# Kernel optimization log

Hardware: AMD Instinct MI355X
Metric: run time of the kernel (lower is better)

The kernel has to match this reference:

```python
import jax, jax.numpy as jnp
import numpy as np

B, S, D, H, L, V = 2, 512, 1024, 16, 12, 50257
HD = D // H
DFF = 4 * D


def _ln(x, g, b, eps=1e-5):
    m = jnp.mean(x, axis=-1, keepdims=True)
    v = jnp.var(x, axis=-1, keepdims=True)
    return (x - m) * jax.lax.rsqrt(v + eps) * g + b


def setup_inputs() -> dict:
    key = jax.random.key(0)
    ks = jax.random.split(key, 32)
    sc = 0.02
    n = lambda k, shape: (jax.random.normal(k, shape, dtype=jnp.float32) * sc)
    inp = {
        "input_ids": jax.random.randint(ks[0], (B, S), 0, V, dtype=jnp.int64),
        "attention_mask": jnp.ones((B, S), dtype=jnp.float32),
        "image_hidden_states": jax.random.normal(ks[1], (B, D), dtype=jnp.float32),
        # token embedding table (also used for position embeds and tied lm_head, as in source)
        "wte": n(ks[2], (V, D)),
        # feature_space_transformation_nn: Linear(1024,1024) -> ReLU -> Linear(1024,1024)
        "ft_W1": n(ks[3], (D, D)), "ft_b1": jnp.zeros((D,), jnp.float32),
        "ft_W2": n(ks[4], (D, D)), "ft_b2": jnp.zeros((D,), jnp.float32),
        # per-layer params, stacked on leading L dim
        "ln1_g": jnp.ones((L, D), jnp.float32), "ln1_b": jnp.zeros((L, D), jnp.float32),
        "Wattn": n(ks[5], (L, D, 3 * D)), "battn": jnp.zeros((L, 3 * D), jnp.float32),
        "Wuk": n(ks[6], (L, D, D)), "buk": jnp.zeros((L, D), jnp.float32),
        "Wuv": n(ks[7], (L, D, D)), "buv": jnp.zeros((L, D), jnp.float32),
        "Wproj": n(ks[8], (L, D, D)), "bproj": jnp.zeros((L, D), jnp.float32),
        "ln2_g": jnp.ones((L, D), jnp.float32), "ln2_b": jnp.zeros((L, D), jnp.float32),
        "Wfc": n(ks[9], (L, D, DFF)), "bfc": jnp.zeros((L, DFF), jnp.float32),
        "Wfc2": n(ks[10], (L, DFF, D)), "bfc2": jnp.zeros((L, D), jnp.float32),
        "lnf_g": jnp.ones((D,), jnp.float32), "lnf_b": jnp.zeros((D,), jnp.float32),
    }
    return inp


def _forward(input_ids, attention_mask, image_hidden_states, wte,
             ft_W1, ft_b1, ft_W2, ft_b2,
             ln1_g, ln1_b, Wattn, battn, Wuk, buk, Wuv, buv, Wproj, bproj,
             ln2_g, ln2_b, Wfc, bfc, Wfc2, bfc2, lnf_g, lnf_b):
    # image feature transformation: Linear -> ReLU -> Linear
    img = jax.nn.relu(image_hidden_states @ ft_W1 + ft_b1) @ ft_W2 + ft_b2  # [B,D]

    # NOTE: source uses wte (not wpe) for position embeddings — faithful reproduction
    h = wte[input_ids] + wte[jnp.arange(S)][None]  # [B,S,D]

    # extended attention mask with a prepended zero column for the image token
    mask_ext = (1.0 - attention_mask)[:, None, None, :] * -10000.0  # [B,1,1,S]
    mask_ext = jnp.concatenate([jnp.zeros((B, 1, 1, 1), mask_ext.dtype), mask_ext], axis=-1)  # [B,1,1,S+1]

    # causal mask over kv_len=S+1: query i sees keys j <= i+1 (image token always visible)
    causal = jnp.arange(S + 1)[None, :] <= (jnp.arange(S)[:, None] + 1)  # [S,S+1]

    def block(h, p):
        (l1g, l1b, Wa, ba, Wk, bk, Wv, bv, Wp, bp, l2g, l2b, Wf, bf, Wf2, bf2) = p
        x = _ln(h, l1g, l1b)
        qkv = x @ Wa + ba
        q, k, v = jnp.split(qkv, 3, axis=-1)  # each [B,S,D]
        ki = (img @ Wk + bk)[:, None, :]  # [B,1,D]
        vi = (img @ Wv + bv)[:, None, :]
        k = jnp.concatenate([ki, k], axis=1)  # [B,S+1,D]
        v = jnp.concatenate([vi, v], axis=1)
        sh = lambda t, n: t.reshape(B, n, H, HD).transpose(0, 2, 1, 3)
        qh, kh, vh = sh(q, S), sh(k, S + 1), sh(v, S + 1)
        s = jnp.einsum('bhqd,bhkd->bhqk', qh, kh) / jnp.sqrt(jnp.float32(HD))
        s = jnp.where(causal[None, None], s, jnp.float32(-10000.0))
        s = s + mask_ext
        a = jax.nn.softmax(s, axis=-1)
        o = jnp.einsum('bhqk,bhkd->bhqd', a, vh).transpose(0, 2, 1, 3).reshape(B, S, D)
        h = h + (o @ Wp + bp)
        x = _ln(h, l2g, l2b)
        h = h + (jax.nn.gelu(x @ Wf + bf, approximate=True) @ Wf2 + bf2)
        return h, None

    params = (ln1_g, ln1_b, Wattn, battn, Wuk, buk, Wuv, buv, Wproj, bproj,
              ln2_g, ln2_b, Wfc, bfc, Wfc2, bfc2)
    h, _ = jax.lax.scan(block, h, params)
    h = _ln(h, lnf_g, lnf_b)
    return h @ wte.T  # tied lm head -> [B,S,V]


def reference(input_ids, attention_mask, image_hidden_states, wte,
              ft_W1, ft_b1, ft_W2, ft_b2,
              ln1_g, ln1_b, Wattn, battn, Wuk, buk, Wuv, buv, Wproj, bproj,
              ln2_g, ln2_b, Wfc, bfc, Wfc2, bfc2, lnf_g, lnf_b):
    return _forward(input_ids, attention_mask, image_hidden_states, wte,
                    ft_W1, ft_b1, ft_W2, ft_b2,
                    ln1_g, ln1_b, Wattn, battn, Wuk, buk, Wuv, buv, Wproj, bproj,
                    ln2_g, ln2_b, Wfc, bfc, Wfc2, bfc2, lnf_g, lnf_b)
```

## Files before the change

kernel.cpp:

```cpp
#include <hip/hip_runtime.h>
#include <cstdint>


typedef __bf16 bf16x8 __attribute__((ext_vector_type(8)));
typedef __bf16 bf16x4 __attribute__((ext_vector_type(4)));
typedef float  f32x4  __attribute__((ext_vector_type(4)));

#define GLDS16(g, l) __builtin_amdgcn_global_load_lds( \
    (const __attribute__((address_space(1))) unsigned int*)(g), \
    (__attribute__((address_space(3))) unsigned int*)(l), 16, 0, 0)

#define SCHED_FENCE() __builtin_amdgcn_sched_barrier(0)

__device__ __forceinline__ float gelu_f(float x) {
    float u = 1.5957691216057308f * (x + 0.044715f * x * x * x);
    float e = __expf(u);
    float t = 1.0f - 2.0f / (e + 1.0f);
    return 0.5f * x * (1.0f + t);
}

__device__ __forceinline__ int fragoff(int row, int kh, int hi) {
    return row * 64 + ((kh * 32 + hi * 8) ^ ((row & 7) << 3));
}

__device__ __forceinline__ void tcvt_body(
    int id, const float* __restrict__ Wa, const float* __restrict__ Wp,
    const float* __restrict__ Wf, const float* __restrict__ Wf2,
    __bf16* __restrict__ oa, __bf16* __restrict__ op,
    __bf16* __restrict__ of, __bf16* __restrict__ of2, float* tile)
{
    const float* src; __bf16* dst; int K, N, kb, nb;
    if (id < 768)       { src = Wa;  dst = oa;  K = 1024; N = 3072; kb = id & 15; nb = id >> 4; }
    else if (id < 1024) { id -= 768;  src = Wp;  dst = op;  K = 1024; N = 1024; kb = id & 15; nb = id >> 4; }
    else if (id < 2048) { id -= 1024; src = Wf;  dst = of;  K = 1024; N = 4096; kb = id & 15; nb = id >> 4; }
    else                { id -= 2048; src = Wf2; dst = of2; K = 4096; N = 1024; kb = id & 63; nb = id >> 6; }
    const int k0 = kb * 64, n0 = nb * 64;
    const int t = threadIdx.x;
    #pragma unroll
    for (int i = 0; i < 4; i++) {
        int r = i * 16 + (t >> 4), c = (t & 15) * 4;
        float4 v = *reinterpret_cast<const float4*>(src + (long)(k0 + r) * N + n0 + c);
        tile[r * 65 + c] = v.x; tile[r * 65 + c + 1] = v.y;
        tile[r * 65 + c + 2] = v.z; tile[r * 65 + c + 3] = v.w;
    }
    __syncthreads();
    const int nrow = t >> 2, kc = (t & 3) * 16;
    bf16x8 o0, o1;
    #pragma unroll
    for (int i = 0; i < 8; i++) {
        o0[i] = (__bf16)tile[(kc + i) * 65 + nrow];
        o1[i] = (__bf16)tile[(kc + 8 + i) * 65 + nrow];
    }
    *reinterpret_cast<bf16x8*>(dst + (long)(n0 + nrow) * K + k0 + kc)     = o0;
    *reinterpret_cast<bf16x8*>(dst + (long)(n0 + nrow) * K + k0 + kc + 8) = o1;
}

__device__ __forceinline__ void wcvt_body(
    int id, const float* __restrict__ wte, __bf16* __restrict__ out, long nvalid)
{
    long base = (long)id * 8192 + threadIdx.x * 8;
    #pragma unroll
    for (int i = 0; i < 4; i++) {
        long e = base + (long)i * 2048;
        bf16x8 o;
        if (e < nvalid) {
            float4 a = *reinterpret_cast<const float4*>(wte + e);
            float4 b = *reinterpret_cast<const float4*>(wte + e + 4);
            o[0] = (__bf16)a.x; o[1] = (__bf16)a.y; o[2] = (__bf16)a.z; o[3] = (__bf16)a.w;
            o[4] = (__bf16)b.x; o[5] = (__bf16)b.y; o[6] = (__bf16)b.z; o[7] = (__bf16)b.w;
        } else {
            #pragma unroll
            for (int q = 0; q < 8; q++) o[q] = (__bf16)0.f;
        }
        *reinterpret_cast<bf16x8*>(out + e) = o;
    }
}

__global__ __launch_bounds__(256) void tcvt_std(
    const float* __restrict__ Wa, const float* __restrict__ Wp,
    const float* __restrict__ Wf, const float* __restrict__ Wf2,
    __bf16* __restrict__ oa, __bf16* __restrict__ op,
    __bf16* __restrict__ of, __bf16* __restrict__ of2)
{
    __shared__ float tile[64 * 65];
    tcvt_body(blockIdx.x, Wa, Wp, Wf, Wf2, oa, op, of, of2, tile);
}

__global__ __launch_bounds__(256) void wcvt_std(
    const float* __restrict__ wte, __bf16* __restrict__ out, long nvalid)
{
    wcvt_body(blockIdx.x, wte, out, nvalid);
}

__global__ __launch_bounds__(256) void gemv_part(
    const float* __restrict__ x, int xld,
    const float* __restrict__ W, long wzs,
    float* __restrict__ part, int K, int N)
{
    int jb = blockIdx.x, kz = blockIdx.y, z = blockIdx.z;
    int t = threadIdx.x;
    int j = (jb << 6) + (t & 63);
    int g = t >> 6;
    int klen = K / (gridDim.y * 4);
    int kbase = (kz * 4 + g) * klen;
    const float* Wp = W + (long)z * wzs + (long)kbase * N + j;
    const float* x0 = x + kbase;
    const float* x1 = x + xld + kbase;
    float a0 = 0.f, a1 = 0.f;
    for (int k = 0; k < klen; k++) {
        float wv = Wp[(long)k * N];
        a0 += x0[k] * wv;
        a1 += x1[k] * wv;
    }
    __shared__ float r0[4][64], r1[4][64];
    r0[g][t & 63] = a0; r1[g][t & 63] = a1;
    __syncthreads();
    if (t < 64) {
        a0 = r0[0][t] + r0[1][t] + r0[2][t] + r0[3][t];
        a1 = r1[0][t] + r1[1][t] + r1[2][t] + r1[3][t];
        long base = (long)(z * gridDim.y + kz) * 2 * N + (jb << 6) + t;
        part[base]     = a0;
        part[base + N] = a1;
    }
}

__global__ __launch_bounds__(256) void gemv_reduce(
    const float* __restrict__ part, const float* __restrict__ bias, long bzs,
    float* __restrict__ out, int N, int nz, int act)
{
    int idx = blockIdx.x * 256 + threadIdx.x;
    if (idx >= nz * 2 * N) return;
    int j  = idx % N;
    int bz = idx / N;
    int z  = bz >> 1;
    float s = bias[(long)z * bzs + j];
    const float* p = part + ((long)z * 8 * 2 + (bz & 1)) * N + j;
    #pragma unroll
    for (int kz = 0; kz < 8; kz++) s += p[(long)kz * 2 * N];
    if (act) s = fmaxf(s, 0.f);
    out[idx] = s;
}

__global__ __launch_bounds__(256) void gemv_kv_part(
    const float* __restrict__ img,
    const float* __restrict__ Wuk, const float* __restrict__ Wuv,
    float* __restrict__ part)
{
    int jb = blockIdx.x, kz = blockIdx.y, z = blockIdx.z;
    int t = threadIdx.x;
    int j = (jb << 6) + (t & 63);
    int g = t >> 6;
    int kbase = (kz * 4 + g) * 64;
    const float* W = (z < 12) ? (Wuk + (long)z * 1048576) : (Wuv + (long)(z - 12) * 1048576);
    const float* Wp = W + (long)kbase * 1024 + j;
    const float* x0 = img + kbase;
    const float* x1 = img + 1024 + kbase;
    float a0 = 0.f, a1 = 0.f;
    for (int k = 0; k < 64; k++) {
        float wv = Wp[(long)k * 1024];
        a0 += x0[k] * wv;
        a1 += x1[k] * wv;
    }
    __shared__ float r0[4][64], r1[4][64];
    r0[g][t & 63] = a0; r1[g][t & 63] = a1;
    __syncthreads();
    if (t < 64) {
        a0 = r0[0][t] + r0[1][t] + r0[2][t] + r0[3][t];
        a1 = r1[0][t] + r1[1][t] + r1[2][t] + r1[3][t];
        long base = (long)(z * 4 + kz) * 2 * 1024 + (jb << 6) + t;
        part[base]        = a0;
        part[base + 1024] = a1;
    }
}

__global__ __launch_bounds__(256) void gemv_kv_reduce(
    const float* __restrict__ part,
    const float* __restrict__ buk, const float* __restrict__ buv,
    float* __restrict__ imgk, float* __restrict__ imgv)
{
    int idx = blockIdx.x * 256 + threadIdx.x;
    int z = idx >> 11;
    int bsel = (idx >> 10) & 1;
    int j = idx & 1023;
    float s = (z < 12) ? buk[z * 1024 + j] : buv[(z - 12) * 1024 + j];
    const float* p = part + ((long)z * 4 * 2 + bsel) * 1024 + j;
    #pragma unroll
    for (int kz = 0; kz < 4; kz++) s += p[(long)kz * 2 * 1024];
    if (z < 12) imgk[z * 2048 + bsel * 1024 + j] = s;
    else        imgv[(z - 12) * 2048 + bsel * 1024 + j] = s;
}

__global__ __launch_bounds__(256) void embed_ln(
    const int* __restrict__ ids, const float* __restrict__ wte,
    float* __restrict__ h, __bf16* __restrict__ xb,
    const float* __restrict__ g, const float* __restrict__ b)
{
    int row = blockIdx.x;
    int s = row & 511;
    int t = threadIdx.x;
    long id = ids[row];
    float4 v1 = reinterpret_cast<const float4*>(wte + id * 1024)[t];
    float4 v2 = reinterpret_cast<const float4*>(wte + (long)s * 1024)[t];
    float4 v; v.x = v1.x + v2.x; v.y = v1.y + v2.y; v.z = v1.z + v2.z; v.w = v1.w + v2.w;
    reinterpret_cast<float4*>(h + (long)row * 1024)[t] = v;

    float s1 = v.x + v.y + v.z + v.w;
    float s2 = v.x * v.x + v.y * v.y + v.z * v.z + v.w * v.w;
    #pragma unroll
    for (int o = 32; o >= 1; o >>= 1) { s1 += __shfl_xor(s1, o); s2 += __shfl_xor(s2, o); }
    __shared__ float r1[4], r2[4];
    int w = t >> 6;
    if ((t & 63) == 0) { r1[w] = s1; r2[w] = s2; }
    __syncthreads();
    s1 = r1[0] + r1[1] + r1[2] + r1[3];
    s2 = r2[0] + r2[1] + r2[2] + r2[3];
    float mean = s1 * (1.0f / 1024.0f);
    float var  = s2 * (1.0f / 1024.0f) - mean * mean;
    float rstd = rsqrtf(var + 1e-5f);
    float4 gg = reinterpret_cast<const float4*>(g)[t];
    float4 bb = reinterpret_cast<const float4*>(b)[t];
    bf16x4 o;
    o[0] = (__bf16)((v.x - mean) * rstd * gg.x + bb.x);
    o[1] = (__bf16)((v.y - mean) * rstd * gg.y + bb.y);
    o[2] = (__bf16)((v.z - mean) * rstd * gg.z + bb.z);
    o[3] = (__bf16)((v.w - mean) * rstd * gg.w + bb.w);
    *reinterpret_cast<bf16x4*>(xb + (long)row * 1024 + t * 4) = o;
}

__global__ __launch_bounds__(256) void ln_k(
    const float* __restrict__ in, __bf16* __restrict__ out,
    const float* __restrict__ g, const float* __restrict__ b)
{
    int row = blockIdx.x, t = threadIdx.x;
    float4 v = reinterpret_cast<const float4*>(in + (long)row * 1024)[t];
    float s1 = v.x + v.y + v.z + v.w;
    float s2 = v.x * v.x + v.y * v.y + v.z * v.z + v.w * v.w;
    #pragma unroll
    for (int o = 32; o >= 1; o >>= 1) { s1 += __shfl_xor(s1, o); s2 += __shfl_xor(s2, o); }
    __shared__ float r1[4], r2[4];
    int w = t >> 6;
    if ((t & 63) == 0) { r1[w] = s1; r2[w] = s2; }
    __syncthreads();
    s1 = r1[0] + r1[1] + r1[2] + r1[3];
    s2 = r2[0] + r2[1] + r2[2] + r2[3];
    float mean = s1 * (1.0f / 1024.0f);
    float var  = s2 * (1.0f / 1024.0f) - mean * mean;
    float rstd = rsqrtf(var + 1e-5f);
    float4 gg = reinterpret_cast<const float4*>(g)[t];
    float4 bb = reinterpret_cast<const float4*>(b)[t];
    bf16x4 o;
    o[0] = (__bf16)((v.x - mean) * rstd * gg.x + bb.x);
    o[1] = (__bf16)((v.y - mean) * rstd * gg.y + bb.y);
    o[2] = (__bf16)((v.z - mean) * rstd * gg.z + bb.z);
    o[3] = (__bf16)((v.w - mean) * rstd * gg.w + bb.w);
    *reinterpret_cast<bf16x4*>(out + (long)row * 1024 + t * 4) = o;
}

template<int NP>
__global__ __launch_bounds__(256) void lnadd_k(
    float* __restrict__ h, const float* __restrict__ part,
    const float* __restrict__ bias,
    const float* __restrict__ g, const float* __restrict__ b,
    __bf16* __restrict__ out)
{
    int row = blockIdx.x, t = threadIdx.x;
    long off = (long)row * 1024 + t * 4;
    float4 v = *reinterpret_cast<const float4*>(h + off);
    #pragma unroll
    for (int sp = 0; sp < NP; sp++) {
        float4 pv = *reinterpret_cast<const float4*>(part + sp * 1048576L + off);
        v.x += pv.x; v.y += pv.y; v.z += pv.z; v.w += pv.w;
    }
    float4 bi = reinterpret_cast<const float4*>(bias)[t];
    v.x += bi.x; v.y += bi.y; v.z += bi.z; v.w += bi.w;
    *reinterpret_cast<float4*>(h + off) = v;

    float s1 = v.x + v.y + v.z + v.w;
    float s2 = v.x * v.x + v.y * v.y + v.z * v.z + v.w * v.w;
    #pragma unroll
    for (int o = 32; o >= 1; o >>= 1) { s1 += __shfl_xor(s1, o); s2 += __shfl_xor(s2, o); }
    __shared__ float r1[4], r2[4];
    int w = t >> 6;
    if ((t & 63) == 0) { r1[w] = s1; r2[w] = s2; }
    __syncthreads();
    s1 = r1[0] + r1[1] + r1[2] + r1[3];
    s2 = r2[0] + r2[1] + r2[2] + r2[3];
    float mean = s1 * (1.0f / 1024.0f);
    float var  = s2 * (1.0f / 1024.0f) - mean * mean;
    float rstd = rsqrtf(var + 1e-5f);
    float4 gg = reinterpret_cast<const float4*>(g)[t];
    float4 bb = reinterpret_cast<const float4*>(b)[t];
    bf16x4 o;
    o[0] = (__bf16)((v.x - mean) * rstd * gg.x + bb.x);
    o[1] = (__bf16)((v.y - mean) * rstd * gg.y + bb.y);
    o[2] = (__bf16)((v.z - mean) * rstd * gg.z + bb.z);
    o[3] = (__bf16)((v.w - mean) * rstd * gg.w + bb.w);
    *reinterpret_cast<bf16x4*>(out + off) = o;
}

__shared__ __bf16 lm8_lds_dummy_decl_guard[1];

__global__ __launch_bounds__(512, 2) void gemm_lm8(
    const __bf16* __restrict__ A, const __bf16* __restrict__ Bt,
    float* __restrict__ C, int N, int K, int GM, int GN)
{
    __shared__ __bf16 lds[65536];
    const int total = GM * GN;
    const int q = total >> 3, r = total & 7;
    const int x = blockIdx.x & 7, jj = blockIdx.x >> 3;
    const int w0 = (x < r) ? x * (q + 1) + jj : r * (q + 1) + (x - r) * q + jj;
    const int m0 = (w0 % GM) * 256;
    const int n0 = (w0 / GM) * 256;

    const int t = threadIdx.x;
    const int wid = t >> 6, lane = t & 63;
    const int lo = lane & 15, hi = lane >> 4;
    const int wr = wid >> 2, wc = wid & 3;

    f32x4 acc[8][4] = {};

    const int srow = t >> 3;
    const int skx  = (((t & 7) ^ (srow & 7)) << 3);
    const int sdst = t * 8;

#define A_OFF(db, hf) ((db) * 16384 + (hf) * 8192)
#define B_OFF(db, hf) (32768 + (db) * 16384 + (hf) * 8192)
#define STAGE_H(db, hsel, kt) do { \
    const int h_ = (hsel) & 1; \
    const __bf16* base_ = ((hsel) < 2) ? (A + (long)(m0 + h_ * 128) * K) \
                                       : (Bt + (long)(n0 + h_ * 128) * K); \
    const int d_ = ((hsel) < 2) ? A_OFF(db, h_) : B_OFF(db, h_); \
    GLDS16(base_ + (long)srow * K + (kt) * 64 + skx,        &lds[d_ + sdst]); \
    GLDS16(base_ + (long)(64 + srow) * K + (kt) * 64 + skx, &lds[d_ + 4096 + sdst]); \
} while (0)

#define PH(db, m, n, DOSTAGE) do { \
    bf16x8 af_[4][2], bf_[2][2]; \
    _Pragma("unroll") \
    for (int mi = 0; mi < 4; mi++) \
        _Pragma("unroll") \
        for (int kh = 0; kh < 2; kh++) \
            af_[mi][kh] = *reinterpret_cast<const bf16x8*>( \
                &lds[A_OFF(db, wr) + fragoff(((m) * 4 + mi) * 16 + lo, kh, hi)]); \
    _Pragma("unroll") \
    for (int ni = 0; ni < 2; ni++) \
        _Pragma("unroll") \
        for (int kh = 0; kh < 2; kh++) \
            bf_[ni][kh] = *reinterpret_cast<const bf16x8*>( \
                &lds[B_OFF(db, wc >> 1) + fragoff((wc & 1) * 64 + ((n) * 2 + ni) * 16 + lo, kh, hi)]); \
    DOSTAGE; \
    asm volatile("s_waitcnt lgkmcnt(0)" ::: "memory"); \
    SCHED_FENCE(); \
    __builtin_amdgcn_s_setprio(1); \
    _Pragma("unroll") \
    for (int mi = 0; mi < 4; mi++) \
        _Pragma("unroll") \
        for (int ni = 0; ni < 2; ni++) \
            _Pragma("unroll") \
            for (int kh = 0; kh < 2; kh++) \
                acc[(m) * 4 + mi][(n) * 2 + ni] = __builtin_amdgcn_mfma_f32_16x16x32_bf16( \
                    af_[mi][kh], bf_[ni][kh], acc[(m) * 4 + mi][(n) * 2 + ni], 0, 0, 0); \
    __builtin_amdgcn_s_setprio(0); \
} while (0)

    const int NKT = K >> 6;
    STAGE_H(0, 0, 0); STAGE_H(0, 1, 0); STAGE_H(0, 2, 0); STAGE_H(0, 3, 0);

    for (int i = 0; i < NKT / 2; i++) {
        const int kt1 = 2 * i + 1, ktn = 2 * i + 2;
        STAGE_H(1, 0, kt1);
        asm volatile("s_waitcnt vmcnt(2)" ::: "memory");
        SCHED_FENCE();
        __builtin_amdgcn_s_barrier();
        SCHED_FENCE();
        PH(0, 0, 0, (void)0);
        PH(0, 0, 1, STAGE_H(1, 1, kt1));
        PH(0, 1, 0, STAGE_H(1, 2, kt1));
        PH(0, 1, 1, STAGE_H(1, 3, kt1));
        SCHED_FENCE();
        __builtin_amdgcn_s_barrier();
        SCHED_FENCE();
        if (ktn < NKT) {
            STAGE_H(0, 0, ktn);
            asm volatile("s_waitcnt vmcnt(2)" ::: "memory");
        } else {
            asm volatile("s_waitcnt vmcnt(0)" ::: "memory");
        }
        SCHED_FENCE();
        __builtin_amdgcn_s_barrier();
        SCHED_FENCE();
        PH(1, 0, 0, (void)0);
        PH(1, 0, 1, if (ktn < NKT) STAGE_H(0, 1, ktn));
        PH(1, 1, 0, if (ktn < NKT) STAGE_H(0, 2, ktn));
        PH(1, 1, 1, if (ktn < NKT) STAGE_H(0, 3, ktn));
        SCHED_FENCE();
        __builtin_amdgcn_s_barrier();
        SCHED_FENCE();
    }
#undef PH
#undef STAGE_H
#undef A_OFF
#undef B_OFF

    #pragma unroll
    for (int mi = 0; mi < 8; mi++)
        #pragma unroll
        for (int ni = 0; ni < 4; ni++) {
            int col = n0 + wc * 64 + ni * 16 + lo;
            if (col < N) {
                #pragma unroll
                for (int rr = 0; rr < 4; rr++) {
                    int row = m0 + wr * 128 + mi * 16 + hi * 4 + rr;
                    C[(long)row * N + col] = acc[mi][ni][rr];
                }
            }
        }
}

template<int BN, int OUTBF16, int ACT, int PARTIAL>
__global__ __launch_bounds__(256) void gemm64(
    const __bf16* __restrict__ A, const __bf16* __restrict__ Bt,
    const float* __restrict__ bias, void* __restrict__ C,
    int N, int K, int GM, int GN, int NS)
{
    constexpr int NB = BN / 32;
    constexpr int LP = 2 + NB;
    const int total = GM * GN * NS;
    const int q = total >> 3, r = total & 7;
    const int x = blockIdx.x & 7, jj = blockIdx.x >> 3;
    const int w0 = (x < r) ? x * (q + 1) + jj : r * (q + 1) + (x - r) * q + jj;
    const int sp = w0 / (GM * GN);
    const int rem = w0 - sp * (GM * GN);
    const int m0 = (rem % GM) * 64;
    const int n0 = (rem / GM) * BN;

    __shared__ __bf16 As[3][64 * 64];
    __shared__ __bf16 Bs[3][BN * 64];
    const int t = threadIdx.x;
    const int wv = t >> 6, lane = t & 63;
    const int lo = lane & 15, hi = lane >> 4;
    const int wr = wv >> 1, wc = wv & 1;

    f32x4 acc[2][NB] = {};

    const int srow = t >> 3;
    const int skx  = (((t & 7) ^ (srow & 7)) << 3);
    const int sldst = t * 8;
    #define ST64(bf, kk) do { \
        _Pragma("unroll") \
        for (int i = 0; i < 2; i++) \
            GLDS16(A + (long)(m0 + i * 32 + srow) * K + (kk) + skx, &As[bf][i * 2048 + sldst]); \
        _Pragma("unroll") \
        for (int i = 0; i < NB; i++) \
            GLDS16(Bt + (long)(n0 + i * 32 + srow) * K + (kk) + skx, &Bs[bf][i * 2048 + sldst]); \
    } while (0)

    const int Ksp = K / NS;
    const int kbeg = sp * Ksp;
    const int T = Ksp >> 6;

    ST64(0, kbeg);
    if (T > 1) ST64(1, kbeg + 64);
    int bcur = 0;
    for (int it = 0; it < T; it++) {
        if (it + 2 < T) {
            int bst = bcur >= 1 ? bcur - 1 : bcur + 2;
            ST64(bst, kbeg + (it + 2) * 64);
            asm volatile("s_waitcnt vmcnt(%0)" :: "i"(2 * LP) : "memory");
        } else if (it + 1 < T) {
            asm volatile("s_waitcnt vmcnt(%0)" :: "i"(LP) : "memory");
        } else {
            asm volatile("s_waitcnt vmcnt(0)" ::: "memory");
        }
        SCHED_FENCE();
        __builtin_amdgcn_s_barrier();
        SCHED_FENCE();

        #pragma unroll
        for (int kh = 0; kh < 2; kh++) {
            bf16x8 afr[2], bfr[NB];
            #pragma unroll
            for (int mi = 0; mi < 2; mi++)
                afr[mi] = *reinterpret_cast<const bf16x8*>(&As[bcur][fragoff(wr * 32 + mi * 16 + lo, kh, hi)]);
            #pragma unroll
            for (int ni = 0; ni < NB; ni++)
                bfr[ni] = *reinterpret_cast<const bf16x8*>(&Bs[bcur][fragoff(wc * (BN / 2) + ni * 16 + lo, kh, hi)]);
            __builtin_amdgcn_s_setprio(1);
            #pragma unroll
            for (int mi = 0; mi < 2; mi++)
                #pragma unroll
                for (int ni = 0; ni < NB; ni++)
                    acc[mi][ni] = __builtin_amdgcn_mfma_f32_16x16x32_bf16(afr[mi], bfr[ni], acc[mi][ni], 0, 0, 0);
            __builtin_amdgcn_s_setprio(0);
        }

        SCHED_FENCE();
        __builtin_amdgcn_s_barrier();
        SCHED_FENCE();
        bcur = bcur < 2 ? bcur + 1 : 0;
    }
    #undef ST64

    const long coff = PARTIAL ? (long)sp * GM * 64 * N : 0;
    #pragma unroll
    for (int mi = 0; mi < 2; mi++)
        #pragma unroll
        for (int ni = 0; ni < NB; ni++) {
            int col = n0 + wc * (BN / 2) + ni * 16 + lo;
            float bv = (!PARTIAL && bias) ? bias[col] : 0.f;
            #pragma unroll
            for (int rr = 0; rr < 4; rr++) {
                int row = m0 + wr * 32 + mi * 16 + hi * 4 + rr;
                float v = acc[mi][ni][rr] + bv;
                if (ACT) v = gelu_f(v);
                if (OUTBF16) ((__bf16*)C)[(long)row * N + col] = (__bf16)v;
                else         ((float*)C)[coff + (long)row * N + col] = v;
            }
        }
}

template<int OUTBF16, int ACT, int RES>
__global__ __launch_bounds__(256) void gemm_bb(
    const __bf16* __restrict__ A, const __bf16* __restrict__ Bt,
    const float* __restrict__ bias, const float* __restrict__ res,
    void* __restrict__ C, int N, int K)
{
    __shared__ __bf16 As[64 * 32];
    __shared__ __bf16 Bs[64 * 32];
    const int t = threadIdx.x;
    const int m0 = blockIdx.x * 64;
    const int n0 = blockIdx.y * 64;
    const int w = t >> 6, lane = t & 63;
    const int lo = lane & 15, hi = lane >> 4;
    const int wr = w >> 1, wc = w & 1;

    f32x4 acc[2][2] = {};

    for (int k0 = 0; k0 < K; k0 += 32) {
        __syncthreads();
        GLDS16(A  + (long)(m0 + (t >> 2)) * K + k0 + ((t & 3) << 3), &As[t * 8]);
        GLDS16(Bt + (long)(n0 + (t >> 2)) * K + k0 + ((t & 3) << 3), &Bs[t * 8]);
        __syncthreads();
        bf16x8 afr[2], bfr[2];
        #pragma unroll
        for (int mi = 0; mi < 2; mi++)
            afr[mi] = *reinterpret_cast<const bf16x8*>(&As[(wr * 32 + mi * 16 + lo) * 32 + hi * 8]);
        #pragma unroll
        for (int ni = 0; ni < 2; ni++)
            bfr[ni] = *reinterpret_cast<const bf16x8*>(&Bs[(wc * 32 + ni * 16 + lo) * 32 + hi * 8]);
        #pragma unroll
        for (int mi = 0; mi < 2; mi++)
            #pragma unroll
            for (int ni = 0; ni < 2; ni++)
                acc[mi][ni] = __builtin_amdgcn_mfma_f32_16x16x32_bf16(afr[mi], bfr[ni], acc[mi][ni], 0, 0, 0);
    }

    #pragma unroll
    for (int mi = 0; mi < 2; mi++)
        #pragma unroll
        for (int ni = 0; ni < 2; ni++) {
            int col = n0 + wc * 32 + ni * 16 + lo;
            float bv = bias ? bias[col] : 0.f;
            #pragma unroll
            for (int rr = 0; rr < 4; rr++) {
                int row = m0 + wr * 32 + mi * 16 + hi * 4 + rr;
                float v = acc[mi][ni][rr] + bv;
                if (ACT) v = gelu_f(v);
                if (RES) v += res[(long)row * N + col];
                if (OUTBF16) ((__bf16*)C)[(long)row * N + col] = (__bf16)v;
                else         ((float*)C)[(long)row * N + col] = v;
            }
        }
}

__global__ __launch_bounds__(256) void gemm_lm(
    const __bf16* __restrict__ A, const float* __restrict__ Wt,
    float* __restrict__ C, int N, int K)
{
    __shared__ __bf16 As[128 * 32];
    __shared__ __bf16 Bs[128 * 32];
    const int t = threadIdx.x;
    const int m0 = blockIdx.x * 128;
    const int n0 = blockIdx.y * 128;
    const int w = t >> 6, lane = t & 63;
    const int lo = lane & 15, hi = lane >> 4;
    const int wr = w >> 1, wc = w & 1;

    f32x4 acc[4][4] = {};

    for (int k0 = 0; k0 < K; k0 += 32) {
        __syncthreads();
        #pragma unroll
        for (int i = 0; i < 2; i++) {
            int c = i * 256 + t;
            GLDS16(A + (long)(m0 + (c >> 2)) * K + k0 + ((c & 3) << 3), &As[c * 8]);
        }
        #pragma unroll
        for (int i = 0; i < 2; i++) {
            int c = i * 256 + t;
            int nr = n0 + (c >> 2);
            bf16x8 bv;
            if (nr < N) {
                const float* wp = Wt + (long)nr * K + k0 + ((c & 3) << 3);
                float4 b0 = *reinterpret_cast<const float4*>(wp);
                float4 b1 = *reinterpret_cast<const float4*>(wp + 4);
                bv[0] = (__bf16)b0.x; bv[1] = (__bf16)b0.y; bv[2] = (__bf16)b0.z; bv[3] = (__bf16)b0.w;
                bv[4] = (__bf16)b1.x; bv[5] = (__bf16)b1.y; bv[6] = (__bf16)b1.z; bv[7] = (__bf16)b1.w;
            } else {
                #pragma unroll
                for (int qq = 0; qq < 8; qq++) bv[qq] = (__bf16)0.f;
            }
            *reinterpret_cast<bf16x8*>(&Bs[c * 8]) = bv;
        }
        __syncthreads();
        bf16x8 afr[4], bfr[4];
        #pragma unroll
        for (int mi = 0; mi < 4; mi++)
            afr[mi] = *reinterpret_cast<const bf16x8*>(&As[(wr * 64 + mi * 16 + lo) * 32 + hi * 8]);
        #pragma unroll
        for (int ni = 0; ni < 4; ni++)
            bfr[ni] = *reinterpret_cast<const bf16x8*>(&Bs[(wc * 64 + ni * 16 + lo) * 32 + hi * 8]);
        #pragma unroll
        for (int mi = 0; mi < 4; mi++)
            #pragma unroll
            for (int ni = 0; ni < 4; ni++)
                acc[mi][ni] = __builtin_amdgcn_mfma_f32_16x16x32_bf16(afr[mi], bfr[ni], acc[mi][ni], 0, 0, 0);
    }

    #pragma unroll
    for (int mi = 0; mi < 4; mi++)
        #pragma unroll
        for (int ni = 0; ni < 4; ni++) {
            int col = n0 + wc * 64 + ni * 16 + lo;
            if (col < N) {
                #pragma unroll
                for (int rr = 0; rr < 4; rr++) {
                    int row = m0 + wr * 64 + mi * 16 + hi * 4 + rr;
                    C[(long)row * N + col] = acc[mi][ni][rr];
                }
            }
        }
}

__global__ __launch_bounds__(256) void attn_aux(
    const __bf16* __restrict__ qkv,
    const float* __restrict__ imgk, const float* __restrict__ imgv,
    const float* __restrict__ amask, __bf16* __restrict__ out,
    int aux_mode,
    const float* __restrict__ Wa, const float* __restrict__ Wp,
    const float* __restrict__ Wf, const float* __restrict__ Wf2,
    __bf16* __restrict__ oa, __bf16* __restrict__ op,
    __bf16* __restrict__ of, __bf16* __restrict__ of2,
    const float* __restrict__ wte, __bf16* __restrict__ wteb, long nvalid)
{
    __shared__ __align__(16) char smem[28416];
    const int bid = blockIdx.x;
    if (bid >= 256) {
        if (aux_mode == 1)
            tcvt_body(bid - 256, Wa, Wp, Wf, Wf2, oa, op, of, of2, (float*)smem);
        else
            wcvt_body(bid - 256, wte, wteb, nvalid);
        return;
    }

    __bf16 (*Ks)[72] = (__bf16(*)[72])(smem);
    __bf16 (*Vt)[72] = (__bf16(*)[72])(smem + 9216);
    __bf16 (*Ps)[16][72] = (__bf16(*)[16][72])(smem + 18432);
    float* kimg_s = (float*)(smem + 27648);
    float* amv_s  = (float*)(smem + 27904);

    const int qb = bid & 7;
    const int h  = (bid >> 3) & 15;
    const int b  = bid >> 7;
    const int t = threadIdx.x, w = t >> 6, lane = t & 63;
    const int lo = lane & 15, hi = lane >> 4;

    const int kr8 = t >> 2, kd8 = (t & 3) * 16;
    const int vr8 = t & 63, vd8 = (t >> 6) * 16;

    const __bf16* qrow = qkv + (long)(b * 512 + qb * 64 + w * 16 + lo) * 3072 + h * 64;
    bf16x8 qf0 = *reinterpret_cast<const bf16x8*>(qrow + hi * 8);
    bf16x8 qf1 = *reinterpret_cast<const bf16x8*>(qrow + 32 + hi * 8);

    if (t < 64) kimg_s[t] = imgk[b * 1024 + h * 64 + t];
    __syncthreads();

    float simg = 0.f;
    #pragma unroll
    for (int i = 0; i < 8; i++)
        simg += (float)qf0[i] * kimg_s[hi * 8 + i] + (float)qf1[i] * kimg_s[32 + hi * 8 + i];
    simg += __shfl_xor(simg, 16);
    simg += __shfl_xor(simg, 32);
    simg *= 0.125f;

    float pimg[4], l_part[4];
    f32x4 o_acc[4];
    #pragma unroll
    for (int rr = 0; rr < 4; rr++) {
        pimg[rr] = __expf(__shfl(simg, hi * 4 + rr));
        l_part[rr] = 0.f;
    }
    #pragma unroll
    for (int df = 0; df < 4; df++) {
        float vi = imgv[b * 1024 + h * 64 + df * 16 + lo];
        #pragma unroll
        for (int rr = 0; rr < 4; rr++) o_acc[df][rr] = pimg[rr] * vi;
    }

    bf16x8 ck0, ck1, cv0, cv1;
    {
        const __bf16* ks = qkv + (long)(b * 512 + kr8) * 3072 + 1024 + h * 64 + kd8;
        ck0 = *reinterpret_cast<const bf16x8*>(ks);
        ck1 = *reinterpret_cast<const bf16x8*>(ks + 8);
        const __bf16* vs = qkv + (long)(b * 512 + vr8) * 3072 + 2048 + h * 64 + vd8;
        cv0 = *reinterpret_cast<const bf16x8*>(vs);
        cv1 = *reinterpret_cast<const bf16x8*>(vs + 8);
    }

    for (int kb = 0; kb <= qb; kb++) {
        bf16x8 nk0, nk1, nv0, nv1;
        const bool more = (kb < qb);
        if (more) {
            const __bf16* ks = qkv + (long)(b * 512 + (kb + 1) * 64 + kr8) * 3072 + 1024 + h * 64 + kd8;
            nk0 = *reinterpret_cast<const bf16x8*>(ks);
            nk1 = *reinterpret_cast<const bf16x8*>(ks + 8);
            const __bf16* vs = qkv + (long)(b * 512 + (kb + 1) * 64 + vr8) * 3072 + 2048 + h * 64 + vd8;
            nv0 = *reinterpret_cast<const bf16x8*>(vs);
            nv1 = *reinterpret_cast<const bf16x8*>(vs + 8);
        }
        __syncthreads();
        *reinterpret_cast<bf16x8*>(&Ks[kr8][kd8])     = ck0;
        *reinterpret_cast<bf16x8*>(&Ks[kr8][kd8 + 8]) = ck1;
        #pragma unroll
        for (int i = 0; i < 8; i++) { Vt[vd8 + i][vr8] = cv0[i]; Vt[vd8 + 8 + i][vr8] = cv1[i]; }
        if (t < 64) amv_s[t] = (1.0f - amask[b * 512 + kb * 64 + t]) * -10000.0f;
        __syncthreads();

        f32x4 sf[4];
        #pragma unroll
        for (int js = 0; js < 4; js++) {
            bf16x8 kf0 = *reinterpret_cast<const bf16x8*>(&Ks[js * 16 + lo][hi * 8]);
            bf16x8 kf1 = *reinterpret_cast<const bf16x8*>(&Ks[js * 16 + lo][32 + hi * 8]);
            f32x4 a = {};
            a = __builtin_amdgcn_mfma_f32_16x16x32_bf16(qf0, kf0, a, 0, 0, 0);
            a = __builtin_amdgcn_mfma_f32_16x16x32_bf16(qf1, kf1, a, 0, 0, 0);
            sf[js] = a;
        }
        #pragma unroll
        for (int js = 0; js < 4; js++) {
            float amv = amv_s[js * 16 + lo];
            #pragma unroll
            for (int rr = 0; rr < 4; rr++) {
                float sv = sf[js][rr] * 0.125f + amv;
                if (kb == qb) {
                    int qrw = w * 16 + hi * 4 + rr;
                    if (js * 16 + lo > qrw) sv = -10000.0f + amv;
                }
                float p = __expf(sv);
                l_part[rr] += p;
                Ps[w][hi * 4 + rr][js * 16 + lo] = (__bf16)p;
            }
        }
        #pragma unroll
        for (int jb = 0; jb < 2; jb++) {
            bf16x8 pf = *reinterpret_cast<const bf16x8*>(&Ps[w][lo][jb * 32 + hi * 8]);
            #pragma unroll
            for (int df = 0; df < 4; df++) {
                bf16x8 vf = *reinterpret_cast<const bf16x8*>(&Vt[df * 16 + lo][jb * 32 + hi * 8]);
                o_acc[df] = __builtin_amdgcn_mfma_f32_16x16x32_bf16(pf, vf, o_acc[df], 0, 0, 0);
            }
        }
        if (more) { ck0 = nk0; ck1 = nk1; cv0 = nv0; cv1 = nv1; }
    }

    float linv[4];
    #pragma unroll
    for (int rr = 0; rr < 4; rr++) {
        float ls = l_part[rr];
        #pragma unroll
        for (int off = 1; off < 16; off <<= 1) ls += __shfl_xor(ls, off);
        linv[rr] = 1.0f / (pimg[rr] + ls);
    }
    #pragma unroll
    for (int df = 0; df < 4; df++)
        #pragma unroll
        for (int rr = 0; rr < 4; rr++) {
            long row = b * 512 + qb * 64 + w * 16 + hi * 4 + rr;
            out[row * 1024 + h * 64 + df * 16 + lo] = (__bf16)(o_acc[df][rr] * linv[rr]);
        }
}

extern "C" void kernel_launch(void* const* d_in, const int* in_sizes, int n_in,
                              void* d_out, int out_size, void* d_ws, size_t ws_size,
                              hipStream_t stream) {
    (void)in_sizes; (void)n_in; (void)out_size;
    const int*   ids   = (const int*)d_in[0];
    const float* amask = (const float*)d_in[1];
    const float* ihs   = (const float*)d_in[2];
    const float* wte   = (const float*)d_in[3];
    const float* ftW1  = (const float*)d_in[4];
    const float* ftb1  = (const float*)d_in[5];
    const float* ftW2  = (const float*)d_in[6];
    const float* ftb2  = (const float*)d_in[7];
    const float* ln1g  = (const float*)d_in[8];
    const float* ln1b  = (const float*)d_in[9];
    const float* Wattn = (const float*)d_in[10];
    const float* battn = (const float*)d_in[11];
    const float* Wuk   = (const float*)d_in[12];
    const float* buk   = (const float*)d_in[13];
    const float* Wuv   = (const float*)d_in[14];
    const float* buv   = (const float*)d_in[15];
    const float* Wproj = (const float*)d_in[16];
    const float* bproj = (const float*)d_in[17];
    const float* ln2g  = (const float*)d_in[18];
    const float* ln2b  = (const float*)d_in[19];
    const float* Wfc   = (const float*)d_in[20];
    const float* bfc   = (const float*)d_in[21];
    const float* Wfc2  = (const float*)d_in[22];
    const float* bfc2  = (const float*)d_in[23];
    const float* lnfg  = (const float*)d_in[24];
    const float* lnfb  = (const float*)d_in[25];
    float* out = (float*)d_out;

    const long VP2 = 50432;
    const long NVALID = 50257L * 1024;
    char* base = (char*)d_ws;
    float* ftmp  = (float*)(base);
    float* img   = (float*)(base + (1 << 13));
    float* imgk  = (float*)(base + (1 << 14));
    float* imgv  = (float*)(base + 114688);
    float* part  = (float*)(base + 212992);
    float* h     = (float*)(base + 1048576);
    char* p = base + 5 * 1048576;
    __bf16* xb    = (__bf16*)p; p += 2 * 1048576;
    __bf16* qkvb  = (__bf16*)p; p += 6 * 1048576;
    __bf16* attob = (__bf16*)p; p += 2 * 1048576;
    __bf16* ffb   = (__bf16*)p; p += 8 * 1048576;
    __bf16* wtA0  = (__bf16*)p; p += 6 * 1048576;
    __bf16* wtP0  = (__bf16*)p; p += 2 * 1048576;
    __bf16* wtF0  = (__bf16*)p; p += 8 * 1048576;
    __bf16* wtF20 = (__bf16*)p; p += 8 * 1048576;
    __bf16* wteb  = (__bf16*)p; p += VP2 * 1024 * 2;
    size_t need1 = (size_t)(p - base);
    float* part_g = (float*)(base + need1);
    size_t need2 = need1 + 4 * 1048576 * sizeof(float);
    char* p2 = base + need2;
    __bf16* wtA1  = (__bf16*)p2; p2 += 6 * 1048576;
    __bf16* wtP1  = (__bf16*)p2; p2 += 2 * 1048576;
    __bf16* wtF1  = (__bf16*)p2; p2 += 8 * 1048576;
    __bf16* wtF21 = (__bf16*)p2; p2 += 8 * 1048576;
    size_t need3 = (size_t)(p2 - base);
    const bool big1 = (ws_size >= need1);
    const bool big2 = (ws_size >= need2);
    const bool big3 = (ws_size >= need3);

    __bf16* wtA_s[2]  = {wtA0, wtA1};
    __bf16* wtP_s[2]  = {wtP0, wtP1};
    __bf16* wtF_s[2]  = {wtF0, wtF1};
    __bf16* wtF2_s[2] = {wtF20, wtF21};

    dim3 b256(256);

    gemv_part<<<dim3(16, 8, 1), b256, 0, stream>>>(ihs, 1024, ftW1, 0, part, 1024, 1024);
    gemv_reduce<<<dim3(8), b256, 0, stream>>>(part, ftb1, 0, ftmp, 1024, 1, 1);
    gemv_part<<<dim3(16, 8, 1), b256, 0, stream>>>(ftmp, 1024, ftW2, 0, part, 1024, 1024);
    gemv_reduce<<<dim3(8), b256, 0, stream>>>(part, ftb2, 0, img, 1024, 1, 0);
    gemv_kv_part<<<dim3(16, 4, 24), b256, 0, stream>>>(img, Wuk, Wuv, part);
    gemv_kv_reduce<<<dim3(192), b256, 0, stream>>>(part, buk, buv, imgk, imgv);

    embed_ln<<<dim3(1024), b256, 0, stream>>>(ids, wte, h, xb, ln1g, ln1b);
    tcvt_std<<<dim3(3072), b256, 0, stream>>>(
        Wattn, Wproj, Wfc, Wfc2, wtA0, wtP0, wtF0, wtF20);

    for (int l = 0; l < 12; l++) {
        const int cs = big3 ? (l & 1) : 0;
        __bf16* cA  = wtA_s[cs];
        __bf16* cP  = wtP_s[cs];
        __bf16* cF  = wtF_s[cs];
        __bf16* cF2 = wtF2_s[cs];

        if (!big3 && l > 0) {
            tcvt_std<<<dim3(3072), b256, 0, stream>>>(
                Wattn + (long)l * 1024 * 3072, Wproj + (long)l * 1024 * 1024,
                Wfc + (long)l * 1024 * 4096, Wfc2 + (long)l * 4096 * 1024,
                wtA0, wtP0, wtF0, wtF20);
        }

        gemm64<128, 1, 0, 0><<<dim3(384), b256, 0, stream>>>(
            xb, cA, battn + l * 3072, qkvb, 3072, 1024, 16, 24, 1);

        if (big3 && l < 11) {
            const int ns = (l + 1) & 1;
            attn_aux<<<dim3(256 + 3072), b256, 0, stream>>>(
                qkvb, imgk + l * 2048, imgv + l * 2048, amask, attob, 1,
                Wattn + (long)(l + 1) * 1024 * 3072, Wproj + (long)(l + 1) * 1024 * 1024,
                Wfc + (long)(l + 1) * 1024 * 4096, Wfc2 + (long)(l + 1) * 4096 * 1024,
                wtA_s[ns], wtP_s[ns], wtF_s[ns], wtF2_s[ns],
                nullptr, nullptr, 0);
        } else if (big3 && l == 11) {
            attn_aux<<<dim3(256 + 6304), b256, 0, stream>>>(
                qkvb, imgk + l * 2048, imgv + l * 2048, amask, attob, 2,
                nullptr, nullptr, nullptr, nullptr,
                nullptr, nullptr, nullptr, nullptr,
                wte, wteb, NVALID);
        } else {
            attn_aux<<<dim3(256), b256, 0, stream>>>(
                qkvb, imgk + l * 2048, imgv + l * 2048, amask, attob, 0,
                nullptr, nullptr, nullptr, nullptr,
                nullptr, nullptr, nullptr, nullptr,
                nullptr, nullptr, 0);
        }

        const float* ng = (l < 11) ? (ln1g + (l + 1) * 1024) : lnfg;
        const float* nb = (l < 11) ? (ln1b + (l + 1) * 1024) : lnfb;
        if (big2) {
            gemm64<64, 0, 0, 1><<<dim3(512), b256, 0, stream>>>(
                attob, cP, nullptr, part_g, 1024, 1024, 16, 16, 2);
            lnadd_k<2><<<dim3(1024), b256, 0, stream>>>(
                h, part_g, bproj + l * 1024, ln2g + l * 1024, ln2b + l * 1024, xb);
            gemm64<128, 1, 1, 0><<<dim3(512), b256, 0, stream>>>(
                xb, cF, bfc + l * 4096, ffb, 4096, 1024, 16, 32, 1);
            gemm64<128, 0, 0, 1><<<dim3(512), b256, 0, stream>>>(
                ffb, cF2, nullptr, part_g, 1024, 4096, 16, 8, 4);
            lnadd_k<4><<<dim3(1024), b256, 0, stream>>>(
                h, part_g, bfc2 + l * 1024, ng, nb, xb);
        } else {
            gemm_bb<0, 0, 1><<<dim3(16, 16), b256, 0, stream>>>(
                attob, cP, bproj + l * 1024, h, h, 1024, 1024);
            ln_k<<<dim3(1024), b256, 0, stream>>>(h, xb, ln2g + l * 1024, ln2b + l * 1024);
            gemm64<128, 1, 1, 0><<<dim3(512), b256, 0, stream>>>(
                xb, cF, bfc + l * 4096, ffb, 4096, 1024, 16, 32, 1);
            gemm_bb<0, 0, 1><<<dim3(16, 16), b256, 0, stream>>>(
                ffb, cF2, bfc2 + l * 1024, h, h, 1024, 4096);
            ln_k<<<dim3(1024), b256, 0, stream>>>(h, xb, ng, nb);
        }
    }

    if (big1) {
        if (!big3)
            wcvt_std<<<dim3((unsigned)(VP2 * 1024 / 8192)), b256, 0, stream>>>(wte, wteb, NVALID);
        gemm_lm8<<<dim3(4 * (int)(VP2 / 256)), dim3(512), 0, stream>>>(
            xb, wteb, out, 50257, 1024, 4, (int)(VP2 / 256));
    } else {
        gemm_lm<<<dim3(8, 393), b256, 0, stream>>>(xb, wte, out, 50257, 1024);
    }
}
```

Measured before the change: 1.447 ms.

## Fuse pre-loop kernels and retile LM head GEMM to 256x128 tiles

Measured after the change: 1.450 ms. Within noise of the previous version (+0.2%).

```diff
diff --git a/kernel.cpp b/kernel.cpp
--- a/kernel.cpp
+++ b/kernel.cpp
@@ -74,6 +74,89 @@
         }
         *reinterpret_cast<bf16x8*>(out + e) = o;
     }
+}
+
+__device__ __forceinline__ void embed_body(
+    int row, const int* __restrict__ ids, const float* __restrict__ wte,
+    float* __restrict__ h, __bf16* __restrict__ xb,
+    const float* __restrict__ g, const float* __restrict__ b, float* red)
+{
+    int s = row & 511;
+    int t = threadIdx.x;
+    long id = ids[row];
+    float4 v1 = reinterpret_cast<const float4*>(wte + id * 1024)[t];
+    float4 v2 = reinterpret_cast<const float4*>(wte + (long)s * 1024)[t];
+    float4 v; v.x = v1.x + v2.x; v.y = v1.y + v2.y; v.z = v1.z + v2.z; v.w = v1.w + v2.w;
+    reinterpret_cast<float4*>(h + (long)row * 1024)[t] = v;
+
+    float s1 = v.x + v.y + v.z + v.w;
+    float s2 = v.x * v.x + v.y * v.y + v.z * v.z + v.w * v.w;
+    #pragma unroll
+    for (int o = 32; o >= 1; o >>= 1) { s1 += __shfl_xor(s1, o); s2 += __shfl_xor(s2, o); }
+    int w = t >> 6;
+    if ((t & 63) == 0) { red[w] = s1; red[4 + w] = s2; }
+    __syncthreads();
+    s1 = red[0] + red[1] + red[2] + red[3];
+    s2 = red[4] + red[5] + red[6] + red[7];
+    float mean = s1 * (1.0f / 1024.0f);
+    float var  = s2 * (1.0f / 1024.0f) - mean * mean;
+    float rstd = rsqrtf(var + 1e-5f);
+    float4 gg = reinterpret_cast<const float4*>(g)[t];
+    float4 bb = reinterpret_cast<const float4*>(b)[t];
+    bf16x4 o;
+    o[0] = (__bf16)((v.x - mean) * rstd * gg.x + bb.x);
+    o[1] = (__bf16)((v.y - mean) * rstd * gg.y + bb.y);
+    o[2] = (__bf16)((v.z - mean) * rstd * gg.z + bb.z);
+    o[3] = (__bf16)((v.w - mean) * rstd * gg.w + bb.w);
+    *reinterpret_cast<bf16x4*>(xb + (long)row * 1024 + t * 4) = o;
+}
+
+__device__ __forceinline__ void ftpart_body(
+    int id, const float* __restrict__ x, const float* __restrict__ W,
+    float* __restrict__ part, float* red)
+{
+    int jb = id & 15, kz = id >> 4;
+    int t = threadIdx.x;
+    int j = (jb << 6) + (t & 63);
+    int g = t >> 6;
+    int kbase = (kz * 4 + g) * 32;
+    const float* Wp = W + (long)kbase * 1024 + j;
+    const float* x0 = x + kbase;
+    const float* x1 = x + 1024 + kbase;
+    float a0 = 0.f, a1 = 0.f;
+    for (int k = 0; k < 32; k++) {
+        float wv = Wp[(long)k * 1024];
+        a0 += x0[k] * wv;
+        a1 += x1[k] * wv;
+    }
+    red[g * 64 + (t & 63)] = a0;
+    red[256 + g * 64 + (t & 63)] = a1;
+    __syncthreads();
+    if (t < 64) {
+        a0 = red[t] + red[64 + t] + red[128 + t] + red[192 + t];
+        a1 = red[256 + t] + red[320 + t] + red[384 + t] + red[448 + t];
+        long base = (long)kz * 2 * 1024 + (jb << 6) + t;
+        part[base]        = a0;
+        part[base + 1024] = a1;
+    }
+}
+
+__global__ __launch_bounds__(256) void preloop0(
+    const int* __restrict__ ids, const float* __restrict__ wte,
+    float* __restrict__ h, __bf16* __restrict__ xb,
+    const float* __restrict__ g, const float* __restrict__ b,
+    const float* __restrict__ Wa, const float* __restrict__ Wp,
+    const float* __restrict__ Wf, const float* __restrict__ Wf2,
+    __bf16* __restrict__ oa, __bf16* __restrict__ op,
+    __bf16* __restrict__ of, __bf16* __restrict__ of2,
+    const float* __restrict__ ihs, const float* __restrict__ ftW1,
+    float* __restrict__ part)
+{
+    __shared__ __align__(16) char smem[16640];
+    const int bid = blockIdx.x;
+    if (bid < 1024)       embed_body(bid, ids, wte, h, xb, g, b, (float*)smem);
+    else if (bid < 4096)  tcvt_body(bid - 1024, Wa, Wp, Wf, Wf2, oa, op, of, of2, (float*)smem);
+    else                  ftpart_body(bid - 4096, ihs, ftW1, part, (float*)smem);
 }
 
 __global__ __launch_bounds__(256) void tcvt_std(
@@ -188,43 +271,6 @@
     for (int kz = 0; kz < 4; kz++) s += p[(long)kz * 2 * 1024];
     if (z < 12) imgk[z * 2048 + bsel * 1024 + j] = s;
     else        imgv[(z - 12) * 2048 + bsel * 1024 + j] = s;
-}
-
-__global__ __launch_bounds__(256) void embed_ln(
-    const int* __restrict__ ids, const float* __restrict__ wte,
-    float* __restrict__ h, __bf16* __restrict__ xb,
-    const float* __restrict__ g, const float* __restrict__ b)
-{
-    int row = blockIdx.x;
-    int s = row & 511;
-    int t = threadIdx.x;
-    long id = ids[row];
-    float4 v1 = reinterpret_cast<const float4*>(wte + id * 1024)[t];
-    float4 v2 = reinterpret_cast<const float4*>(wte + (long)s * 1024)[t];
-    float4 v; v.x = v1.x + v2.x; v.y = v1.y + v2.y; v.z = v1.z + v2.z; v.w = v1.w + v2.w;
-    reinterpret_cast<float4*>(h + (long)row * 1024)[t] = v;
-
-    float s1 = v.x + v.y + v.z + v.w;
-    float s2 = v.x * v.x + v.y * v.y + v.z * v.z + v.w * v.w;
-    #pragma unroll
-    for (int o = 32; o >= 1; o >>= 1) { s1 += __shfl_xor(s1, o); s2 += __shfl_xor(s2, o); }
-    __shared__ float r1[4], r2[4];
-    int w = t >> 6;
-    if ((t & 63) == 0) { r1[w] = s1; r2[w] = s2; }
-    __syncthreads();
-    s1 = r1[0] + r1[1] + r1[2] + r1[3];
-    s2 = r2[0] + r2[1] + r2[2] + r2[3];
-    float mean = s1 * (1.0f / 1024.0f);
-    float var  = s2 * (1.0f / 1024.0f) - mean * mean;
-    float rstd = rsqrtf(var + 1e-5f);
-    float4 gg = reinterpret_cast<const float4*>(g)[t];
-    float4 bb = reinterpret_cast<const float4*>(b)[t];
-    bf16x4 o;
-    o[0] = (__bf16)((v.x - mean) * rstd * gg.x + bb.x);
-    o[1] = (__bf16)((v.y - mean) * rstd * gg.y + bb.y);
-    o[2] = (__bf16)((v.z - mean) * rstd * gg.z + bb.z);
-    o[3] = (__bf16)((v.w - mean) * rstd * gg.w + bb.w);
-    *reinterpret_cast<bf16x4*>(xb + (long)row * 1024 + t * 4) = o;
 }
 
 __global__ __launch_bounds__(256) void ln_k(
@@ -298,56 +344,54 @@
     *reinterpret_cast<bf16x4*>(out + off) = o;
 }
 
-__shared__ __bf16 lm8_lds_dummy_decl_guard[1];
-
-__global__ __launch_bounds__(512, 2) void gemm_lm8(
+__global__ __launch_bounds__(512) void gemm_lm8b(
     const __bf16* __restrict__ A, const __bf16* __restrict__ Bt,
     float* __restrict__ C, int N, int K, int GM, int GN)
 {
-    __shared__ __bf16 lds[65536];
+    __shared__ __bf16 lds[49152];
     const int total = GM * GN;
     const int q = total >> 3, r = total & 7;
     const int x = blockIdx.x & 7, jj = blockIdx.x >> 3;
     const int w0 = (x < r) ? x * (q + 1) + jj : r * (q + 1) + (x - r) * q + jj;
     const int m0 = (w0 % GM) * 256;
-    const int n0 = (w0 / GM) * 256;
+    const int n0 = (w0 / GM) * 128;
 
     const int t = threadIdx.x;
     const int wid = t >> 6, lane = t & 63;
     const int lo = lane & 15, hi = lane >> 4;
     const int wr = wid >> 2, wc = wid & 3;
 
-    f32x4 acc[8][4] = {};
+    f32x4 acc[8][2] = {};
 
     const int srow = t >> 3;
     const int skx  = (((t & 7) ^ (srow & 7)) << 3);
     const int sdst = t * 8;
 
-#define A_OFF(db, hf) ((db) * 16384 + (hf) * 8192)
-#define B_OFF(db, hf) (32768 + (db) * 16384 + (hf) * 8192)
-#define STAGE_H(db, hsel, kt) do { \
-    const int h_ = (hsel) & 1; \
-    const __bf16* base_ = ((hsel) < 2) ? (A + (long)(m0 + h_ * 128) * K) \
-                                       : (Bt + (long)(n0 + h_ * 128) * K); \
-    const int d_ = ((hsel) < 2) ? A_OFF(db, h_) : B_OFF(db, h_); \
-    GLDS16(base_ + (long)srow * K + (kt) * 64 + skx,        &lds[d_ + sdst]); \
-    GLDS16(base_ + (long)(64 + srow) * K + (kt) * 64 + skx, &lds[d_ + 4096 + sdst]); \
+#define ST_A(db, hf, kt) do { \
+    const __bf16* b_ = A + (long)(m0 + (hf) * 128) * K + (long)(kt) * 64; \
+    GLDS16(b_ + (long)srow * K + skx,        &lds[(db) * 16384 + (hf) * 8192 + sdst]); \
+    GLDS16(b_ + (long)(64 + srow) * K + skx, &lds[(db) * 16384 + (hf) * 8192 + 4096 + sdst]); \
 } while (0)
-
-#define PH(db, m, n, DOSTAGE) do { \
+#define ST_B(db, kt) do { \
+    const __bf16* b_ = Bt + (long)n0 * K + (long)(kt) * 64; \
+    GLDS16(b_ + (long)srow * K + skx,        &lds[32768 + (db) * 8192 + sdst]); \
+    GLDS16(b_ + (long)(64 + srow) * K + skx, &lds[32768 + (db) * 8192 + 4096 + sdst]); \
+} while (0)
+
+#define PHB(db, mq, DOSTAGE) do { \
     bf16x8 af_[4][2], bf_[2][2]; \
     _Pragma("unroll") \
     for (int mi = 0; mi < 4; mi++) \
         _Pragma("unroll") \
         for (int kh = 0; kh < 2; kh++) \
             af_[mi][kh] = *reinterpret_cast<const bf16x8*>( \
-                &lds[A_OFF(db, wr) + fragoff(((m) * 4 + mi) * 16 + lo, kh, hi)]); \
+                &lds[(db) * 16384 + wr * 8192 + fragoff(((mq) * 4 + mi) * 16 + lo, kh, hi)]); \
     _Pragma("unroll") \
     for (int ni = 0; ni < 2; ni++) \
         _Pragma("unroll") \
         for (int kh = 0; kh < 2; kh++) \
             bf_[ni][kh] = *reinterpret_cast<const bf16x8*>( \
-                &lds[B_OFF(db, wc >> 1) + fragoff((wc & 1) * 64 + ((n) * 2 + ni) * 16 + lo, kh, hi)]); \
+                &lds[32768 + (db) * 8192 + fragoff(wc * 32 + ni * 16 + lo, kh, hi)]); \
     DOSTAGE; \
     asm volatile("s_waitcnt lgkmcnt(0)" ::: "memory"); \
     SCHED_FENCE(); \
@@ -358,55 +402,41 @@
         for (int ni = 0; ni < 2; ni++) \
             _Pragma("unroll") \
             for (int kh = 0; kh < 2; kh++) \
-                acc[(m) * 4 + mi][(n) * 2 + ni] = __builtin_amdgcn_mfma_f32_16x16x32_bf16( \
-                    af_[mi][kh], bf_[ni][kh], acc[(m) * 4 + mi][(n) * 2 + ni], 0, 0, 0); \
+                acc[(mq) * 4 + mi][ni] = __builtin_amdgcn_mfma_f32_16x16x32_bf16( \
+                    af_[mi][kh], bf_[ni][kh], acc[(mq) * 4 + mi][ni], 0, 0, 0); \
     __builtin_amdgcn_s_setprio(0); \
 } while (0)
 
     const int NKT = K >> 6;
-    STAGE_H(0, 0, 0); STAGE_H(0, 1, 0); STAGE_H(0, 2, 0); STAGE_H(0, 3, 0);
-
-    for (int i = 0; i < NKT / 2; i++) {
-        const int kt1 = 2 * i + 1, ktn = 2 * i + 2;
-        STAGE_H(1, 0, kt1);
-        asm volatile("s_waitcnt vmcnt(2)" ::: "memory");
+    ST_A(0, 0, 0); ST_A(0, 1, 0); ST_B(0, 0);
+
+    for (int kt = 0; kt < NKT; kt++) {
+        const int db = kt & 1;
+        const bool more = (kt + 1 < NKT);
+        if (more) {
+            ST_A(db ^ 1, 0, kt + 1);
+            asm volatile("s_waitcnt vmcnt(2)" ::: "memory");
+        } else {
+            asm volatile("s_waitcnt vmcnt(0)" ::: "memory");
+        }
         SCHED_FENCE();
         __builtin_amdgcn_s_barrier();
         SCHED_FENCE();
-        PH(0, 0, 0, (void)0);
-        PH(0, 0, 1, STAGE_H(1, 1, kt1));
-        PH(0, 1, 0, STAGE_H(1, 2, kt1));
-        PH(0, 1, 1, STAGE_H(1, 3, kt1));
+        PHB(db, 0, if (more) ST_A(db ^ 1, 1, kt + 1));
+        PHB(db, 1, if (more) ST_B(db ^ 1, kt + 1));
         SCHED_FENCE();
         __builtin_amdgcn_s_barrier();
         SCHED_FENCE();
-        if (ktn < NKT) {
-            STAGE_H(0, 0, ktn);
-            asm volatile("s_waitcnt vmcnt(2)" ::: "memory");
-        } else {
-            asm volatile("s_waitcnt vmcnt(0)" ::: "memory");
-        }
-        SCHED_FENCE();
-        __builtin_amdgcn_s_barrier();
-        SCHED_FENCE();
-        PH(1, 0, 0, (void)0);
-        PH(1, 0, 1, if (ktn < NKT) STAGE_H(0, 1, ktn));
-        PH(1, 1, 0, if (ktn < NKT) STAGE_H(0, 2, ktn));
-        PH(1, 1, 1, if (ktn < NKT) STAGE_H(0, 3, ktn));
-        SCHED_FENCE();
-        __builtin_amdgcn_s_barrier();
-        SCHED_FENCE();
-    }
-#undef PH
-#undef STAGE_H
-#undef A_OFF
-#undef B_OFF
+    }
+#undef PHB
+#undef ST_A
+#undef ST_B
 
     #pragma unroll
     for (int mi = 0; mi < 8; mi++)
         #pragma unroll
-        for (int ni = 0; ni < 4; ni++) {
-            int col = n0 + wc * 64 + ni * 16 + lo;
+        for (int ni = 0; ni < 2; ni++) {
+            int col = n0 + wc * 32 + ni * 16 + lo;
             if (col < N) {
                 #pragma unroll
                 for (int rr = 0; rr < 4; rr++) {
@@ -861,16 +891,15 @@
 
     dim3 b256(256);
 
-    gemv_part<<<dim3(16, 8, 1), b256, 0, stream>>>(ihs, 1024, ftW1, 0, part, 1024, 1024);
+    preloop0<<<dim3(4224), b256, 0, stream>>>(
+        ids, wte, h, xb, ln1g, ln1b,
+        Wattn, Wproj, Wfc, Wfc2, wtA0, wtP0, wtF0, wtF20,
+        ihs, ftW1, part);
     gemv_reduce<<<dim3(8), b256, 0, stream>>>(part, ftb1, 0, ftmp, 1024, 1, 1);
     gemv_part<<<dim3(16, 8, 1), b256, 0, stream>>>(ftmp, 1024, ftW2, 0, part, 1024, 1024);
     gemv_reduce<<<dim3(8), b256, 0, stream>>>(part, ftb2, 0, img, 1024, 1, 0);
     gemv_kv_part<<<dim3(16, 4, 24), b256, 0, stream>>>(img, Wuk, Wuv, part);
     gemv_kv_reduce<<<dim3(192), b256, 0, stream>>>(part, buk, buv, imgk, imgv);
-
-    embed_ln<<<dim3(1024), b256, 0, stream>>>(ids, wte, h, xb, ln1g, ln1b);
-    tcvt_std<<<dim3(3072), b256, 0, stream>>>(
-        Wattn, Wproj, Wfc, Wfc2, wtA0, wtP0, wtF0, wtF20);
 
     for (int l = 0; l < 12; l++) {
         const int cs = big3 ? (l & 1) : 0;
@@ -939,8 +968,8 @@
     if (big1) {
         if (!big3)
             wcvt_std<<<dim3((unsigned)(VP2 * 1024 / 8192)), b256, 0, stream>>>(wte, wteb, NVALID);
-        gemm_lm8<<<dim3(4 * (int)(VP2 / 256)), dim3(512), 0, stream>>>(
-            xb, wteb, out, 50257, 1024, 4, (int)(VP2 / 256));
+        gemm_lm8b<<<dim3(4 * (int)(VP2 / 128)), dim3(512), 0, stream>>>(
+            xb, wteb, out, 50257, 1024, 4, (int)(VP2 / 128));
     } else {
         gemm_lm<<<dim3(8, 393), b256, 0, stream>>>(xb, wte, out, 50257, 1024);
     }
```
